# Kernel optimization log

Measured on AMD Instinct MI355X. Metric: run time of the kernel, lower is better.

The kernel has to match this reference:

```python
import jax, jax.numpy as jnp
import numpy as np

N_NODES = 100000
N_EDGES = 1600000
HIDDEN = 64
FILTERS = 64
GAUSS = 5
SHORT = 5
N_CONV = 2
Z_DIM = 2 * FILTERS + SHORT  # CGConv concat [x_i, x_j, e]


def setup_inputs() -> dict:
    key = jax.random.key(0)
    ks = jax.random.split(key, 12)
    h = jax.random.normal(ks[0], (N_NODES, HIDDEN), dtype=jnp.float32)
    edge_index = jax.random.randint(ks[1], (2, N_EDGES), 0, N_NODES, dtype=jnp.int64)
    edge_weight = jax.random.uniform(ks[2], (N_EDGES,), dtype=jnp.float32)
    edge_attr = jax.random.uniform(ks[3], (N_EDGES, GAUSS), dtype=jnp.float32)
    s = 1.0 / np.sqrt(HIDDEN)
    lin0_w = jax.random.uniform(ks[4], (HIDDEN, FILTERS), jnp.float32, -s, s)
    lin0_b = jax.random.uniform(ks[5], (FILTERS,), jnp.float32, -s, s)
    s2 = 1.0 / np.sqrt(GAUSS)
    short_w = jax.random.uniform(ks[6], (GAUSS, SHORT), jnp.float32, -s2, s2)
    short_b = jax.random.uniform(ks[7], (SHORT,), jnp.float32, -s2, s2)
    s3 = 1.0 / np.sqrt(Z_DIM)
    conv_f_w = jax.random.uniform(ks[8], (N_CONV, Z_DIM, FILTERS), jnp.float32, -s3, s3)
    conv_f_b = jax.random.uniform(ks[9], (N_CONV, FILTERS), jnp.float32, -s3, s3)
    conv_s_w = jax.random.uniform(ks[10], (N_CONV, Z_DIM, FILTERS), jnp.float32, -s3, s3)
    conv_s_b = jax.random.uniform(ks[11], (N_CONV, FILTERS), jnp.float32, -s3, s3)
    return {
        'h': h, 'edge_index': edge_index, 'edge_weight': edge_weight,
        'edge_attr': edge_attr, 'data': 0,
        'lin0_w': lin0_w, 'lin0_b': lin0_b,
        'short_w': short_w, 'short_b': short_b,
        'conv_f_w': conv_f_w, 'conv_f_b': conv_f_b,
        'conv_s_w': conv_s_w, 'conv_s_b': conv_s_b,
    }


def _cgconv(x, src, dst, e, wf, bf, ws, bs):
    # z = [x_i, x_j, e]; split the matmul to avoid materializing z[E, 2F+5]
    x_i = x[dst]  # target node features [E, F]
    x_j = x[src]  # source node features [E, F]
    F_ = x.shape[1]
    zf = x_i @ wf[:F_] + x_j @ wf[F_:2 * F_] + e @ wf[2 * F_:] + bf
    zs = x_i @ ws[:F_] + x_j @ ws[F_:2 * F_] + e @ ws[2 * F_:] + bs
    msg = jax.nn.sigmoid(zf) * jax.nn.softplus(zs)  # gated messages [E, F]
    agg = jax.ops.segment_sum(msg, dst, num_segments=x.shape[0])
    return x + agg  # residual, aggr='add', batch_norm=False


def reference(h, edge_index, edge_weight, edge_attr, data,
              lin0_w, lin0_b, short_w, short_b,
              conv_f_w, conv_f_b, conv_s_w, conv_s_b):
    out = jax.nn.relu(h @ lin0_w + lin0_b)          # [N, F]
    e = jax.nn.relu(edge_attr @ short_w + short_b)  # [E, 5]
    src, dst = edge_index[0], edge_index[1]
    for i in range(N_CONV):
        out = jax.nn.relu(_cgconv(out, src, dst, e,
                                  conv_f_w[i], conv_f_b[i],
                                  conv_s_w[i], conv_s_b[i]))
    return out
```

## Files before the change

### kernel.cpp

```cpp
#include <hip/hip_runtime.h>

#define NN 100000
#define NE 1600000
#define NSB 391

#define LOG2E 1.4426950408889634f
#define LN2 0.6931471805599453f

typedef short short4v __attribute__((ext_vector_type(4)));
typedef short short8v __attribute__((ext_vector_type(8)));
typedef float f32x2 __attribute__((ext_vector_type(2)));
typedef float f32x4 __attribute__((ext_vector_type(4)));
typedef unsigned u32x4 __attribute__((ext_vector_type(4)));

static __device__ __forceinline__ unsigned f2bf(float x) {
    unsigned b = __float_as_uint(x);
    return (b + 0x7FFFu + ((b >> 16) & 1u)) >> 16;
}
static __device__ __forceinline__ float bflo(unsigned u) { return __uint_as_float(u << 16); }
static __device__ __forceinline__ float bfhi(unsigned u) { return __uint_as_float(u & 0xFFFF0000u); }
static __device__ __forceinline__ int imin(int a, int b) { return a < b ? a : b; }
static __device__ __forceinline__ short8v mk8(short4v a, short4v b) {
    short8v r;
    r[0] = a[0]; r[1] = a[1]; r[2] = a[2]; r[3] = a[3];
    r[4] = b[0]; r[5] = b[1]; r[6] = b[2]; r[7] = b[3];
    return r;
}

static __device__ __forceinline__ int swz(int row, int colblk) {
    return row * 64 + ((colblk ^ (row & 7)) << 3);
}

static __device__ __forceinline__ void frag_reads(const short* xl, int row, int g,
                                                  short8v& a0, short8v& a1) {
    const int sub = (g & 1) * 4;
    const int cb = g >> 1;
    const short4v p0 = *(const short4v*)&xl[swz(row, cb + 0) + sub];
    const short4v p1 = *(const short4v*)&xl[swz(row, cb + 2) + sub];
    const short4v p2 = *(const short4v*)&xl[swz(row, cb + 4) + sub];
    const short4v p3 = *(const short4v*)&xl[swz(row, cb + 6) + sub];
    a0 = mk8(p0, p1);
    a1 = mk8(p2, p3);
}

static __device__ __forceinline__ float edge_acc(uint4 m, unsigned ps, f32x2 pd2,
                                                 const f32x2* __restrict__ w2, float acc) {
    f32x2 z = __builtin_amdgcn_cvt_pk_f32_fp8((int)ps, false);
    z += pd2;
    const float e50 = bflo(m.y), e51 = bfhi(m.y);
    const float e52 = bflo(m.z), e53 = bfhi(m.z);
    const float e54 = bflo(m.w);
    z += e50 * w2[0];
    z += e51 * w2[1];
    z += e52 * w2[2];
    z += e53 * w2[3];
    z += e54 * w2[4];
    const float sig = __builtin_amdgcn_rcpf(1.f + __builtin_amdgcn_exp2f(z.x));
    const float gg = __builtin_amdgcn_logf(1.f + __builtin_amdgcn_exp2f(z.y));
    return fmaf(sig, gg, acc);
}

__global__ __launch_bounds__(256) void k_wpack(const float* __restrict__ cfw,
                                               const float* __restrict__ csw,
                                               const float* __restrict__ l0w,
                                               unsigned short* __restrict__ Bp) {
    const int qq = blockIdx.x * 256 + threadIdx.x;
    const float* src;
    float scale;
    int roff, ct, kh, l;
    if (qq < 4096) {
        const int layer = qq >> 11;
        const int q = qq & 2047;
        const int m = q >> 9;
        const int rem = q & 511;
        ct = rem >> 7;
        kh = (rem >> 6) & 1;
        l = rem & 63;
        scale = (m & 1) ? LOG2E : -LOG2E;
        src = ((m & 1) ? csw : cfw) + (size_t)layer * 133 * 64;
        roff = (m >> 1) ? 64 : 0;
    } else {
        const int p = qq - 4096;
        ct = p >> 7;
        kh = (p >> 6) & 1;
        l = p & 63;
        scale = 1.f;
        src = l0w;
        roff = 0;
    }
    const int n = ct * 16 + (l & 15);
#pragma unroll
    for (int j = 0; j < 8; j++) {
        const int k = kh * 32 + ((j < 4) ? (4 * (l >> 4) + j) : (16 + 4 * (l >> 4) + j - 4));
        Bp[(size_t)qq * 8 + j] = (unsigned short)f2bf(scale * src[(size_t)(roff + k) * 64 + n]);
    }
}

__global__ __launch_bounds__(256) void k_lin0m_hist(const float* __restrict__ h,
                                                    const unsigned short* __restrict__ Bp0,
                                                    const float* __restrict__ b,
                                                    float* __restrict__ x0,
                                                    unsigned short* __restrict__ xb,
                                                    const int* __restrict__ ei,
                                                    int* __restrict__ cnt,
                                                    int* __restrict__ rank) {
    __shared__ __align__(16) short xl[32 * 64];
    const int r7 = blockIdx.x % 7;
    const int q7 = blockIdx.x / 7;
    if (r7 < 2) {
        const int base = (q7 * 2 + r7) * 1280 + threadIdx.x;
        int r[5];
#pragma unroll
        for (int j = 0; j < 5; j++) r[j] = atomicAdd(&cnt[ei[NE + base + j * 256]], 1);
#pragma unroll
        for (int j = 0; j < 5; j++) rank[base + j * 256] = r[j];
        return;
    }
    const int rowbase = (q7 * 5 + (r7 - 2)) * 32;
    {
        const float4* hs = (const float4*)(h + (size_t)rowbase * 64);
#pragma unroll
        for (int it = 0; it < 2; it++) {
            const int i = threadIdx.x + it * 256;
            const float4 v = hs[i];
            short4v sv;
            sv[0] = (short)f2bf(v.x);
            sv[1] = (short)f2bf(v.y);
            sv[2] = (short)f2bf(v.z);
            sv[3] = (short)f2bf(v.w);
            const int row = i >> 4;
            *(short4v*)&xl[swz(row, (i >> 1) & 7) + (i & 1) * 4] = sv;
        }
    }
    __syncthreads();
    const int ct = threadIdx.x >> 6;
    const int l = threadIdx.x & 63;
    const int lm = l & 15;
    const int g = l >> 4;
    short8v A[2][2];
#pragma unroll
    for (int rt = 0; rt < 2; rt++) frag_reads(xl, rt * 16 + lm, g, A[rt][0], A[rt][1]);
    const short* bp = (const short*)Bp0;
    const short8v B0 = *(const short8v*)&bp[((ct * 2 + 0) * 64 + l) * 8];
    const short8v B1 = *(const short8v*)&bp[((ct * 2 + 1) * 64 + l) * 8];
    const int col = ct * 16 + lm;
    const float bc = b[col];
#pragma unroll
    for (int rt = 0; rt < 2; rt++) {
        f32x4 a = {0.f, 0.f, 0.f, 0.f};
        a = __builtin_amdgcn_mfma_f32_16x16x32_bf16(A[rt][0], B0, a, 0, 0, 0);
        a = __builtin_amdgcn_mfma_f32_16x16x32_bf16(A[rt][1], B1, a, 0, 0, 0);
#pragma unroll
        for (int reg = 0; reg < 4; reg++) {
            const int rowg = rowbase + rt * 16 + g * 4 + reg;
            const float r = fmaxf(a[reg] + bc, 0.f);
            x0[(size_t)rowg * 64 + col] = r;
            xb[(size_t)rowg * 64 + col] = (unsigned short)f2bf(r);
        }
    }
}

__global__ __launch_bounds__(256) void k_scan1(const int* __restrict__ cnt,
                                               int* __restrict__ offs, int* __restrict__ bsum) {
    __shared__ int sm[256];
    const int t = threadIdx.x;
    const int i = blockIdx.x * 256 + t;
    const int v = (i < NN) ? cnt[i] : 0;
    sm[t] = v;
    __syncthreads();
    for (int off = 1; off < 256; off <<= 1) {
        const int x = (t >= off) ? sm[t - off] : 0;
        __syncthreads();
        sm[t] += x;
        __syncthreads();
    }
    if (i < NN) offs[i] = sm[t] - v;
    if (t == 255) bsum[blockIdx.x] = sm[255];
}

__global__ __launch_bounds__(512) void k_scan2(int* __restrict__ bsum) {
    __shared__ int sm[512];
    const int t = threadIdx.x;
    const int v = (t < NSB) ? bsum[t] : 0;
    sm[t] = v;
    __syncthreads();
    for (int off = 1; off < 512; off <<= 1) {
        const int x = (t >= off) ? sm[t - off] : 0;
        __syncthreads();
        sm[t] += x;
        __syncthreads();
    }
    if (t < NSB) bsum[t] = sm[t] - v;
}

__global__ __launch_bounds__(256) void k_scan3(int* __restrict__ offs,
                                               const int* __restrict__ bsum) {
    const int i = blockIdx.x * 256 + threadIdx.x;
    if (i < NN) offs[i] += bsum[blockIdx.x];
    if (i == 0) offs[NN] = NE;
}

__global__ __launch_bounds__(256) void k_scat_proj(const int* __restrict__ ei,
                                                   const float* __restrict__ eattr,
                                                   const float* __restrict__ sw,
                                                   const float* __restrict__ sb,
                                                   const int* __restrict__ rank,
                                                   const int* __restrict__ offs,
                                                   unsigned* __restrict__ meta,
                                                   const unsigned short* __restrict__ xb,
                                                   const unsigned short* __restrict__ Bp,
                                                   const float* __restrict__ bfv,
                                                   const float* __restrict__ bsv,
                                                   unsigned* __restrict__ Pd,
                                                   unsigned short* __restrict__ Ps8) {
    __shared__ __align__(16) short xl[32 * 64];
    const int r7 = blockIdx.x % 7;
    const int q7 = blockIdx.x / 7;
    if (r7 < 2) {
        __shared__ float swl[25], sbl[5];
        if (threadIdx.x < 25) swl[threadIdx.x] = sw[threadIdx.x];
        if (threadIdx.x >= 32 && threadIdx.x < 37) sbl[threadIdx.x - 32] = sb[threadIdx.x - 32];
        __syncthreads();
        const int base = (q7 * 2 + r7) * 1280 + threadIdx.x;
        int s[5], d[5], r[5];
        float ea[5][5];
#pragma unroll
        for (int j = 0; j < 5; j++) {
            const int e = base + j * 256;
            s[j] = ei[e];
            d[j] = ei[NE + e];
            r[j] = rank[e];
#pragma unroll
            for (int k = 0; k < 5; k++) ea[j][k] = eattr[(size_t)e * 5 + k];
        }
        int pos[5];
#pragma unroll
        for (int j = 0; j < 5; j++) pos[j] = offs[d[j]] + r[j];
#pragma unroll
        for (int j = 0; j < 5; j++) {
            unsigned u5[5];
#pragma unroll
            for (int k = 0; k < 5; k++) {
                float a = sbl[k];
#pragma unroll
                for (int q = 0; q < 5; q++) a += ea[j][q] * swl[q * 5 + k];
                u5[k] = f2bf(fmaxf(a, 0.f));
            }
            u32x4 m;
            m[0] = (unsigned)s[j];
            m[1] = u5[0] | (u5[1] << 16);
            m[2] = u5[2] | (u5[3] << 16);
            m[3] = u5[4];
            __builtin_nontemporal_store(m, (u32x4*)&meta[(size_t)pos[j] * 4]);
        }
        return;
    }
    const int rowbase = (q7 * 5 + (r7 - 2)) * 32;
    {
        const u32x4* xsrc = (const u32x4*)(xb + (size_t)rowbase * 64);
        const int i = threadIdx.x;
        const u32x4 v = __builtin_nontemporal_load(&xsrc[i]);
        *(u32x4*)&xl[swz(i >> 3, i & 7)] = v;
    }
    __syncthreads();
    const int ct = threadIdx.x >> 6;
    const int l = threadIdx.x & 63;
    const int lm = l & 15;
    const int g = l >> 4;
    short8v A[2][2];
#pragma unroll
    for (int rt = 0; rt < 2; rt++) frag_reads(xl, rt * 16 + lm, g, A[rt][0], A[rt][1]);
    const short* bp = (const short*)Bp;
    f32x4 acc[4][2];
#pragma unroll
    for (int m = 0; m < 4; m++) {
        const short8v B0 = *(const short8v*)&bp[(((m * 4 + ct) * 2 + 0) * 64 + l) * 8];
        const short8v B1 = *(const short8v*)&bp[(((m * 4 + ct) * 2 + 1) * 64 + l) * 8];
#pragma unroll
        for (int rt = 0; rt < 2; rt++) {
            f32x4 a = {0.f, 0.f, 0.f, 0.f};
            a = __builtin_amdgcn_mfma_f32_16x16x32_bf16(A[rt][0], B0, a, 0, 0, 0);
            a = __builtin_amdgcn_mfma_f32_16x16x32_bf16(A[rt][1], B1, a, 0, 0, 0);
            acc[m][rt] = a;
        }
    }
    const int col = ct * 16 + lm;
    const float bfb = -LOG2E * bfv[col];
    const float bsb = LOG2E * bsv[col];
#pragma unroll
    for (int rt = 0; rt < 2; rt++) {
#pragma unroll
        for (int reg = 0; reg < 4; reg++) {
            const int rowg = rowbase + rt * 16 + g * 4 + reg;
            Pd[(size_t)rowg * 64 + col] =
                f2bf(acc[0][rt][reg] + bfb) | (f2bf(acc[1][rt][reg] + bsb) << 16);
            Ps8[(size_t)rowg * 64 + col] = (unsigned short)__builtin_amdgcn_cvt_pk_fp8_f32(
                acc[2][rt][reg], acc[3][rt][reg], 0, false);
        }
    }
}

__global__ __launch_bounds__(256) void k_projm(const unsigned short* __restrict__ xb,
                                               const unsigned short* __restrict__ Bp,
                                               const float* __restrict__ bfv,
                                               const float* __restrict__ bsv,
                                               unsigned* __restrict__ Pd,
                                               unsigned short* __restrict__ Ps8) {
    __shared__ __align__(16) short xl[32 * 64];
    const int rowbase = blockIdx.x * 32;
    {
        const u32x4* xsrc = (const u32x4*)(xb + (size_t)rowbase * 64);
        const int i = threadIdx.x;
        const u32x4 v = __builtin_nontemporal_load(&xsrc[i]);
        *(u32x4*)&xl[swz(i >> 3, i & 7)] = v;
    }
    __syncthreads();
    const int ct = threadIdx.x >> 6;
    const int l = threadIdx.x & 63;
    const int lm = l & 15;
    const int g = l >> 4;
    short8v A[2][2];
#pragma unroll
    for (int rt = 0; rt < 2; rt++) frag_reads(xl, rt * 16 + lm, g, A[rt][0], A[rt][1]);
    const short* bp = (const short*)Bp;
    f32x4 acc[4][2];
#pragma unroll
    for (int m = 0; m < 4; m++) {
        const short8v B0 = *(const short8v*)&bp[(((m * 4 + ct) * 2 + 0) * 64 + l) * 8];
        const short8v B1 = *(const short8v*)&bp[(((m * 4 + ct) * 2 + 1) * 64 + l) * 8];
#pragma unroll
        for (int rt = 0; rt < 2; rt++) {
            f32x4 a = {0.f, 0.f, 0.f, 0.f};
            a = __builtin_amdgcn_mfma_f32_16x16x32_bf16(A[rt][0], B0, a, 0, 0, 0);
            a = __builtin_amdgcn_mfma_f32_16x16x32_bf16(A[rt][1], B1, a, 0, 0, 0);
            acc[m][rt] = a;
        }
    }
    const int col = ct * 16 + lm;
    const float bfb = -LOG2E * bfv[col];
    const float bsb = LOG2E * bsv[col];
#pragma unroll
    for (int rt = 0; rt < 2; rt++) {
#pragma unroll
        for (int reg = 0; reg < 4; reg++) {
            const int rowg = rowbase + rt * 16 + g * 4 + reg;
            Pd[(size_t)rowg * 64 + col] =
                f2bf(acc[0][rt][reg] + bfb) | (f2bf(acc[1][rt][reg] + bsb) << 16);
            Ps8[(size_t)rowg * 64 + col] = (unsigned short)__builtin_amdgcn_cvt_pk_fp8_f32(
                acc[2][rt][reg], acc[3][rt][reg], 0, false);
        }
    }
}

__global__ __launch_bounds__(64) void k_seg(const int* __restrict__ offs,
                                            const uint4* __restrict__ meta,
                                            const unsigned* __restrict__ Pd,
                                            const unsigned short* __restrict__ Ps8,
                                            const float* __restrict__ wfE,
                                            const float* __restrict__ wsE,
                                            const float* __restrict__ xin,
                                            float* __restrict__ out,
                                            unsigned short* __restrict__ xbout) {
    const int n = blockIdx.x;
    const int lane = threadIdx.x;
    const int start = __builtin_amdgcn_readfirstlane(offs[n]);
    const int end = __builtin_amdgcn_readfirstlane(offs[n + 1]);
    const unsigned pd = __builtin_nontemporal_load(&Pd[(size_t)n * 64 + lane]);
    f32x2 pd2;
    pd2.x = bflo(pd);
    pd2.y = bfhi(pd);
    f32x2 w2[5];
#pragma unroll
    for (int k = 0; k < 5; k++) {
        f32x2 p;
        p.x = -LOG2E * wfE[k * 64 + lane];
        p.y = LOG2E * wsE[k * 64 + lane];
        w2[k] = p;
    }
    const float xv = __builtin_nontemporal_load(&xin[(size_t)n * 64 + lane]);
    float acc = 0.f;
    const int cnt = end - start;
    if (cnt > 0) {
        const int last = end - 1;
        const int nbF = (cnt + 3) >> 2;
        uint4 M0[4], M1[4];
        unsigned PS0[4];
#pragma unroll
        for (int j = 0; j < 4; j++) M0[j] = meta[imin(start + j, last)];
#pragma unroll
        for (int j = 0; j < 4; j++) M1[j] = meta[imin(start + 4 + j, last)];
#pragma unroll
        for (int j = 0; j < 4; j++) PS0[j] = Ps8[(size_t)M0[j].x * 64 + lane];
        for (int b = 0; b < nbF - 1; b++) {
            const int base2 = __builtin_amdgcn_readfirstlane(start + (b + 2) * 4);
            uint4 M2[4];
            unsigned PS1[4];
#pragma unroll
            for (int j = 0; j < 4; j++) M2[j] = meta[imin(base2 + j, last)];
#pragma unroll
            for (int j = 0; j < 4; j++) PS1[j] = Ps8[(size_t)M1[j].x * 64 + lane];
#pragma unroll
            for (int j = 0; j < 4; j++) acc = edge_acc(M0[j], PS0[j], pd2, w2, acc);
#pragma unroll
            for (int j = 0; j < 4; j++) {
                M0[j] = M1[j];
                M1[j] = M2[j];
                PS0[j] = PS1[j];
            }
        }
        const int lb = start + (nbF - 1) * 4;
#pragma unroll
        for (int j = 0; j < 4; j++)
            if (lb + j < end) acc = edge_acc(M0[j], PS0[j], pd2, w2, acc);
    }
    const float res = fmaxf(fmaf(acc, LN2, xv), 0.f);
    if (xbout) {
        out[(size_t)n * 64 + lane] = res;
        xbout[(size_t)n * 64 + lane] = (unsigned short)f2bf(res);
    } else {
        __builtin_nontemporal_store(res, &out[(size_t)n * 64 + lane]);
    }
}

extern "C" void kernel_launch(void* const* d_in, const int* in_sizes, int n_in,
                              void* d_out, int out_size, void* d_ws, size_t ws_size,
                              hipStream_t stream) {
    const float* h = (const float*)d_in[0];
    const int* ei = (const int*)d_in[1];
    const float* eattr = (const float*)d_in[3];
    const float* lin0_w = (const float*)d_in[5];
    const float* lin0_b = (const float*)d_in[6];
    const float* short_w = (const float*)d_in[7];
    const float* short_b = (const float*)d_in[8];
    const float* conv_f_w = (const float*)d_in[9];
    const float* conv_f_b = (const float*)d_in[10];
    const float* conv_s_w = (const float*)d_in[11];
    const float* conv_s_b = (const float*)d_in[12];

    char* ws = (char*)d_ws;
    uint4* meta = (uint4*)ws;
    float* X0 = (float*)(ws + (size_t)NE * 16);
    float* X1 = X0 + (size_t)NN * 64;
    unsigned* Pd = (unsigned*)(X1 + (size_t)NN * 64);
    unsigned short* Ps8 = (unsigned short*)(Pd + (size_t)NN * 64);
    unsigned short* XB = Ps8 + (size_t)NN * 64;
    unsigned short* Bp = XB + (size_t)NN * 64;
    int* cnt = (int*)(Bp + 36864);
    int* offs = cnt + NN;
    int* bsum = offs + NN + 1;
    int* rank = (int*)X1;

    hipMemsetAsync(cnt, 0, (size_t)NN * 4, stream);
    k_wpack<<<18, 256, 0, stream>>>(conv_f_w, conv_s_w, lin0_w, Bp);
    k_lin0m_hist<<<4375, 256, 0, stream>>>(h, Bp + 32768, lin0_b, X0, XB, ei, cnt, rank);
    k_scan1<<<NSB, 256, 0, stream>>>(cnt, offs, bsum);
    k_scan2<<<1, 512, 0, stream>>>(bsum);
    k_scan3<<<NSB, 256, 0, stream>>>(offs, bsum);
    k_scat_proj<<<4375, 256, 0, stream>>>(ei, eattr, short_w, short_b, rank, offs,
                                          (unsigned*)meta, XB, Bp, conv_f_b, conv_s_b,
                                          Pd, Ps8);
    k_seg<<<NN, 64, 0, stream>>>(offs, meta, Pd, Ps8,
                                 conv_f_w + 128 * 64, conv_s_w + 128 * 64,
                                 X0, X1, XB);
    k_projm<<<NN / 32, 256, 0, stream>>>(XB, Bp + 16384, conv_f_b + 64, conv_s_b + 64, Pd, Ps8);
    k_seg<<<NN, 64, 0, stream>>>(offs, meta, Pd, Ps8,
                                 conv_f_w + 133 * 64 + 128 * 64,
                                 conv_s_w + 133 * 64 + 128 * 64,
                                 X1, (float*)d_out, (unsigned short*)nullptr);
}
```

Baseline: 310.1 us.

## Drop fp32 node-feature buffers, keep residual in bf16, pack two nodes per block

Removes the fp32 X0/X1 intermediate node-feature arrays. The residual input is now read from the bf16 XB buffer, and the first conv pass writes only bf16 output in place into XB. This cuts global write and read traffic for node features. The segment kernel also handles two nodes per 128-thread block instead of one per 64-thread block, which reduces block count and launch overhead. The trade-off is that the residual path loses precision because it goes through bf16. Writing XB in place is only safe because each node reads and writes only its own row.

```diff
diff --git a/kernel.cpp b/kernel.cpp
--- a/kernel.cpp
+++ b/kernel.cpp
@@ -99,7 +99,6 @@
 __global__ __launch_bounds__(256) void k_lin0m_hist(const float* __restrict__ h,
                                                     const unsigned short* __restrict__ Bp0,
                                                     const float* __restrict__ b,
-                                                    float* __restrict__ x0,
                                                     unsigned short* __restrict__ xb,
                                                     const int* __restrict__ ei,
                                                     int* __restrict__ cnt,
@@ -153,9 +152,7 @@
 #pragma unroll
         for (int reg = 0; reg < 4; reg++) {
             const int rowg = rowbase + rt * 16 + g * 4 + reg;
-            const float r = fmaxf(a[reg] + bc, 0.f);
-            x0[(size_t)rowg * 64 + col] = r;
-            xb[(size_t)rowg * 64 + col] = (unsigned short)f2bf(r);
+            xb[(size_t)rowg * 64 + col] = (unsigned short)f2bf(fmaxf(a[reg] + bc, 0.f));
         }
     }
 }
@@ -352,17 +349,17 @@
     }
 }
 
-__global__ __launch_bounds__(64) void k_seg(const int* __restrict__ offs,
-                                            const uint4* __restrict__ meta,
-                                            const unsigned* __restrict__ Pd,
-                                            const unsigned short* __restrict__ Ps8,
-                                            const float* __restrict__ wfE,
-                                            const float* __restrict__ wsE,
-                                            const float* __restrict__ xin,
-                                            float* __restrict__ out,
-                                            unsigned short* __restrict__ xbout) {
-    const int n = blockIdx.x;
-    const int lane = threadIdx.x;
+__global__ __launch_bounds__(128) void k_seg(const int* __restrict__ offs,
+                                             const uint4* __restrict__ meta,
+                                             const unsigned* __restrict__ Pd,
+                                             const unsigned short* __restrict__ Ps8,
+                                             const float* __restrict__ wfE,
+                                             const float* __restrict__ wsE,
+                                             const unsigned short* __restrict__ xbin,
+                                             float* __restrict__ outf,
+                                             unsigned short* __restrict__ xbout) {
+    const int n = blockIdx.x * 2 + (threadIdx.x >> 6);
+    const int lane = threadIdx.x & 63;
     const int start = __builtin_amdgcn_readfirstlane(offs[n]);
     const int end = __builtin_amdgcn_readfirstlane(offs[n + 1]);
     const unsigned pd = __builtin_nontemporal_load(&Pd[(size_t)n * 64 + lane]);
@@ -377,7 +374,7 @@
         p.y = LOG2E * wsE[k * 64 + lane];
         w2[k] = p;
     }
-    const float xv = __builtin_nontemporal_load(&xin[(size_t)n * 64 + lane]);
+    const float xv = bflo((unsigned)xbin[(size_t)n * 64 + lane]);
     float acc = 0.f;
     const int cnt = end - start;
     if (cnt > 0) {
@@ -414,11 +411,10 @@
             if (lb + j < end) acc = edge_acc(M0[j], PS0[j], pd2, w2, acc);
     }
     const float res = fmaxf(fmaf(acc, LN2, xv), 0.f);
-    if (xbout) {
-        out[(size_t)n * 64 + lane] = res;
+    if (outf) {
+        __builtin_nontemporal_store(res, &outf[(size_t)n * 64 + lane]);
+    } else {
         xbout[(size_t)n * 64 + lane] = (unsigned short)f2bf(res);
-    } else {
-        __builtin_nontemporal_store(res, &out[(size_t)n * 64 + lane]);
     }
 }
 
@@ -439,32 +435,30 @@
 
     char* ws = (char*)d_ws;
     uint4* meta = (uint4*)ws;
-    float* X0 = (float*)(ws + (size_t)NE * 16);
-    float* X1 = X0 + (size_t)NN * 64;
-    unsigned* Pd = (unsigned*)(X1 + (size_t)NN * 64);
+    unsigned* Pd = (unsigned*)(ws + (size_t)NE * 16);
     unsigned short* Ps8 = (unsigned short*)(Pd + (size_t)NN * 64);
     unsigned short* XB = Ps8 + (size_t)NN * 64;
     unsigned short* Bp = XB + (size_t)NN * 64;
     int* cnt = (int*)(Bp + 36864);
     int* offs = cnt + NN;
     int* bsum = offs + NN + 1;
-    int* rank = (int*)X1;
+    int* rank = bsum + NSB;
 
     hipMemsetAsync(cnt, 0, (size_t)NN * 4, stream);
     k_wpack<<<18, 256, 0, stream>>>(conv_f_w, conv_s_w, lin0_w, Bp);
-    k_lin0m_hist<<<4375, 256, 0, stream>>>(h, Bp + 32768, lin0_b, X0, XB, ei, cnt, rank);
+    k_lin0m_hist<<<4375, 256, 0, stream>>>(h, Bp + 32768, lin0_b, XB, ei, cnt, rank);
     k_scan1<<<NSB, 256, 0, stream>>>(cnt, offs, bsum);
     k_scan2<<<1, 512, 0, stream>>>(bsum);
     k_scan3<<<NSB, 256, 0, stream>>>(offs, bsum);
     k_scat_proj<<<4375, 256, 0, stream>>>(ei, eattr, short_w, short_b, rank, offs,
                                           (unsigned*)meta, XB, Bp, conv_f_b, conv_s_b,
                                           Pd, Ps8);
-    k_seg<<<NN, 64, 0, stream>>>(offs, meta, Pd, Ps8,
-                                 conv_f_w + 128 * 64, conv_s_w + 128 * 64,
-                                 X0, X1, XB);
+    k_seg<<<NN / 2, 128, 0, stream>>>(offs, meta, Pd, Ps8,
+                                      conv_f_w + 128 * 64, conv_s_w + 128 * 64,
+                                      XB, nullptr, XB);
     k_projm<<<NN / 32, 256, 0, stream>>>(XB, Bp + 16384, conv_f_b + 64, conv_s_b + 64, Pd, Ps8);
-    k_seg<<<NN, 64, 0, stream>>>(offs, meta, Pd, Ps8,
-                                 conv_f_w + 133 * 64 + 128 * 64,
-                                 conv_s_w + 133 * 64 + 128 * 64,
-                                 X1, (float*)d_out, (unsigned short*)nullptr);
-}
+    k_seg<<<NN / 2, 128, 0, stream>>>(offs, meta, Pd, Ps8,
+                                      conv_f_w + 133 * 64 + 128 * 64,
+                                      conv_s_w + 133 * 64 + 128 * 64,
+                                      XB, (float*)d_out, nullptr);
+}
```

After: 313.9 us. No clear change (+1.2%).
